# Kernel tuning notes

Measured on AMD Instinct MI355X. Metric: run time of the kernel, lower is better.

Reference implementation:

```python
import jax, jax.numpy as jnp
import numpy as np

H = 1152  # hidden_size
NH = 16   # num_attention_heads
HD = H // NH  # head_dim = 72
FF = 4304  # intermediate_size
EPS = 1e-6
S = 4096
B = 1
NDOCS = 32


def _linear_params(key, d_in, d_out):
    kw, kb = jax.random.split(key)
    lim = 1.0 / np.sqrt(d_in)
    w = jax.random.uniform(kw, (d_out, d_in), jnp.float32, -lim, lim)
    b = jax.random.uniform(kb, (d_out,), jnp.float32, -lim, lim)
    return w, b


def setup_inputs() -> dict:
    key = jax.random.key(0)
    ks = jax.random.split(key, 8)
    hidden_states = jax.random.normal(ks[0], (B, S, H), jnp.float32)
    document_ids = jnp.sort(jax.random.randint(ks[1], (S,), 0, NDOCS))
    q_w, q_b = _linear_params(ks[2], H, H)
    k_w, k_b = _linear_params(ks[3], H, H)
    v_w, v_b = _linear_params(ks[4], H, H)
    o_w, o_b = _linear_params(ks[5], H, H)
    fc1_w, fc1_b = _linear_params(ks[6], H, FF)
    fc2_w, fc2_b = _linear_params(ks[7], FF, H)
    return {
        'hidden_states': hidden_states,
        'document_ids': document_ids,
        'q_w': q_w, 'q_b': q_b, 'k_w': k_w, 'k_b': k_b,
        'v_w': v_w, 'v_b': v_b, 'o_w': o_w, 'o_b': o_b,
        'ln1_g': jnp.ones((H,), jnp.float32), 'ln1_b': jnp.zeros((H,), jnp.float32),
        'ln2_g': jnp.ones((H,), jnp.float32), 'ln2_b': jnp.zeros((H,), jnp.float32),
        'fc1_w': fc1_w, 'fc1_b': fc1_b, 'fc2_w': fc2_w, 'fc2_b': fc2_b,
    }


def _layer_norm(x, g, b):
    mu = jnp.mean(x, axis=-1, keepdims=True)
    var = jnp.mean(jnp.square(x - mu), axis=-1, keepdims=True)
    return (x - mu) * jax.lax.rsqrt(var + EPS) * g + b


def _forward(hidden_states, q_w, q_b, k_w, k_b, v_w, v_b, o_w, o_b,
             ln1_g, ln1_b, ln2_g, ln2_b, fc1_w, fc1_b, fc2_w, fc2_b,
             document_ids):
    b, s, _ = hidden_states.shape
    scale = HD ** -0.5

    residual = hidden_states
    x = _layer_norm(hidden_states, ln1_g, ln1_b)

    # projections (torch Linear: y = x @ W.T + b)
    q = (x @ q_w.T + q_b).reshape(b, s, NH, HD).transpose(0, 2, 1, 3)
    k = (x @ k_w.T + k_b).reshape(b, s, NH, HD).transpose(0, 2, 1, 3)
    v = (x @ v_w.T + v_b).reshape(b, s, NH, HD).transpose(0, 2, 1, 3)

    # document-masked attention: attend only within same document id
    scores = jnp.einsum('bhqd,bhkd->bhqk', q, k) * scale
    mask = document_ids[:, None] == document_ids[None, :]  # [s, s]
    scores = jnp.where(mask[None, None], scores, -jnp.inf)
    attn = jax.nn.softmax(scores, axis=-1)
    out = jnp.einsum('bhqk,bhkd->bhqd', attn, v)  # [b,h,s,d]
    out = out.transpose(0, 2, 1, 3).reshape(b, s, H)
    out = out @ o_w.T + o_b

    hidden = residual + out
    residual = hidden
    x = _layer_norm(hidden, ln2_g, ln2_b)
    x = jax.nn.gelu(x @ fc1_w.T + fc1_b, approximate=True)
    x = x @ fc2_w.T + fc2_b
    return residual + x


def reference(hidden_states, document_ids, q_w, q_b, k_w, k_b, v_w, v_b,
              o_w, o_b, ln1_g, ln1_b, ln2_g, ln2_b, fc1_w, fc1_b, fc2_w, fc2_b):
    return _forward(hidden_states, q_w, q_b, k_w, k_b, v_w, v_b, o_w, o_b,
                    ln1_g, ln1_b, ln2_g, ln2_b, fc1_w, fc1_b, fc2_w, fc2_b,
                    document_ids)
```

## Files before the change

kernel.cpp:

```cpp
#include <hip/hip_runtime.h>

typedef unsigned short u16;
typedef unsigned int u32;
typedef __attribute__((ext_vector_type(8))) __bf16 bf16x8;
typedef __attribute__((ext_vector_type(8))) u16 u16x8;
typedef __attribute__((ext_vector_type(4))) float f32x4;
typedef __attribute__((ext_vector_type(2))) u32 u32x2;

#define SEQ 4096
#define HID 1152
#define NHEAD 16
#define HDIM 72
#define FF 4304
#define FFP 4352
#define H3 3456

__device__ __forceinline__ u16 f2bf(float f) {
  u32 u = __builtin_bit_cast(u32, f);
  u32 r = u + 0x7fffu + ((u >> 16) & 1u);
  return (u16)(r >> 16);
}
__device__ __forceinline__ float bf2f(u16 h) {
  return __builtin_bit_cast(float, (u32)h << 16);
}
__device__ __forceinline__ float bflo(u32 u) { return __builtin_bit_cast(float, u << 16); }
__device__ __forceinline__ float bfhi(u32 u) { return __builtin_bit_cast(float, u & 0xffff0000u); }

typedef const __attribute__((address_space(1))) void* gas_t;
typedef __attribute__((address_space(3))) void* las_t;
__device__ __forceinline__ void load_lds16(const void* g, void* l) {
  __builtin_amdgcn_global_load_lds((gas_t)(unsigned long long)g,
                                   (las_t)(u32)(unsigned long long)l, 16, 0, 0);
}

__device__ __forceinline__ float gelu_fast(float x) {
  float z = 0.7978845608f * (x + 0.044715f * x * x * x);
  return x / (1.f + __expf(-2.f * z));
}

__global__ __launch_bounds__(256) void cvt4x4_k(const float* __restrict__ a,
                                                const float* __restrict__ b,
                                                const float* __restrict__ c,
                                                const float* __restrict__ d,
                                                u16* __restrict__ out, int n4) {
  int i = blockIdx.x * 256 + threadIdx.x;
  if (i >= n4) return;
  const float* in = (blockIdx.y == 0) ? a : (blockIdx.y == 1) ? b : (blockIdx.y == 2) ? c : d;
  f32x4 f = ((const f32x4*)in)[i];
  u32x2 o;
  o[0] = (u32)f2bf(f[0]) | ((u32)f2bf(f[1]) << 16);
  o[1] = (u32)f2bf(f[2]) | ((u32)f2bf(f[3]) << 16);
  ((u32x2*)(out + (size_t)blockIdx.y * n4 * 4))[i] = o;
}

__global__ __launch_bounds__(256) void cvt4_pad_k(const float* __restrict__ in,
                                                  u16* __restrict__ out,
                                                  int rows, int sc, int dc) {
  int i = blockIdx.x * 256 + threadIdx.x;
  long long n4 = (long long)rows * dc / 4;
  if (i >= n4) return;
  long long idx = (long long)i * 4;
  int r = (int)(idx / dc);
  int c = (int)(idx % dc);
  u32x2 o;
  if (c < sc) {
    f32x4 f = *(const f32x4*)(in + (size_t)r * sc + c);
    o[0] = (u32)f2bf(f[0]) | ((u32)f2bf(f[1]) << 16);
    o[1] = (u32)f2bf(f[2]) | ((u32)f2bf(f[3]) << 16);
  } else {
    o[0] = 0; o[1] = 0;
  }
  ((u32x2*)out)[i] = o;
}

__global__ __launch_bounds__(256) void prep_k(const int* __restrict__ ids,
                                              const float* __restrict__ qb,
                                              const float* __restrict__ kb,
                                              const float* __restrict__ vb,
                                              const float* __restrict__ f1b,
                                              int* __restrict__ se,
                                              float* __restrict__ bqkv,
                                              float* __restrict__ bf1,
                                              float* __restrict__ zbuf) {
  int i = blockIdx.x * 256 + threadIdx.x;
  if (i < H3) bqkv[i] = (i < HID) ? qb[i] : (i < 2 * HID ? kb[i - HID] : vb[i - 2 * HID]);
  if (i < FFP) bf1[i] = (i < FF) ? f1b[i] : 0.f;
  if (i < 16) zbuf[i] = 0.f;
  if (i < SEQ) {
    int id = ids[i];
    int lo = 0, hi = SEQ;
    while (lo < hi) { int mid = (lo + hi) >> 1; if (ids[mid] < id) lo = mid + 1; else hi = mid; }
    int s = lo;
    lo = 0; hi = SEQ;
    while (lo < hi) { int mid = (lo + hi) >> 1; if (ids[mid] <= id) lo = mid + 1; else hi = mid; }
    se[2 * i] = s;
    se[2 * i + 1] = lo;
  }
}

__global__ __launch_bounds__(256) void ln_k(const float* __restrict__ x,
                                            const float* __restrict__ g,
                                            const float* __restrict__ b,
                                            u16* __restrict__ y) {
  __shared__ float sred[8];
  int row = blockIdx.x, tid = threadIdx.x;
  const f32x4* xr = (const f32x4*)(x + (size_t)row * HID);
  f32x4 v0 = {}, v1 = {};
  float s = 0.f, s2 = 0.f;
  int c0 = tid, c1 = tid + 256;
  v0 = xr[c0];
  if (c1 < 288) v1 = xr[c1];
#pragma unroll
  for (int j = 0; j < 4; ++j) { s += v0[j] + v1[j]; s2 += v0[j] * v0[j] + v1[j] * v1[j]; }
#pragma unroll
  for (int sh = 32; sh; sh >>= 1) { s += __shfl_xor(s, sh); s2 += __shfl_xor(s2, sh); }
  if ((tid & 63) == 0) { sred[tid >> 6] = s; sred[4 + (tid >> 6)] = s2; }
  __syncthreads();
  s = sred[0] + sred[1] + sred[2] + sred[3];
  s2 = sred[4] + sred[5] + sred[6] + sred[7];
  float mu = s * (1.f / HID);
  float rs = rsqrtf(s2 * (1.f / HID) - mu * mu + 1e-6f);
  u16* yr = y + (size_t)row * HID;
  const f32x4* g4 = (const f32x4*)g;
  const f32x4* b4 = (const f32x4*)b;
  {
    f32x4 gv = g4[c0], bv = b4[c0];
    u32x2 o;
    o[0] = (u32)f2bf((v0[0] - mu) * rs * gv[0] + bv[0]) |
           ((u32)f2bf((v0[1] - mu) * rs * gv[1] + bv[1]) << 16);
    o[1] = (u32)f2bf((v0[2] - mu) * rs * gv[2] + bv[2]) |
           ((u32)f2bf((v0[3] - mu) * rs * gv[3] + bv[3]) << 16);
    *(u32x2*)(yr + c0 * 4) = o;
  }
  if (c1 < 288) {
    f32x4 gv = g4[c1], bv = b4[c1];
    u32x2 o;
    o[0] = (u32)f2bf((v1[0] - mu) * rs * gv[0] + bv[0]) |
           ((u32)f2bf((v1[1] - mu) * rs * gv[1] + bv[1]) << 16);
    o[1] = (u32)f2bf((v1[2] - mu) * rs * gv[2] + bv[2]) |
           ((u32)f2bf((v1[3] - mu) * rs * gv[3] + bv[3]) << 16);
    *(u32x2*)(yr + c1 * 4) = o;
  }
}

template <int EP>
__global__ __launch_bounds__(256, 4) void gemm_bt(const u16* __restrict__ A,
                                                  const u16* __restrict__ B,
                                                  void* __restrict__ outp,
                                                  const float* __restrict__ bias,
                                                  const float* __restrict__ resid,
                                                  int M, int N, int K) {
  __shared__ u16 As[128 * 64];
  __shared__ u16 Bs[128 * 64];
  int tid = threadIdx.x;
  int l = tid & 63, w = tid >> 6;
  int nxy = gridDim.x * gridDim.y;
  int bidf = blockIdx.y * gridDim.x + blockIdx.x;
  int cpx = nxy >> 3;
  bidf = (bidf & 7) * cpx + (bidf >> 3);
  int m0 = (bidf / gridDim.x) * 128;
  int n0 = (bidf % gridDim.x) * 128;
  int wr = w >> 1, wc = w & 1;
  f32x4 acc[4][4] = {};
  int srow = tid >> 3;
  int scol = ((tid & 7) * 16) ^ ((srow & 7) << 4);
  const char* Ab = (const char*)A + ((size_t)(m0 + srow) * K) * 2 + scol;
  const char* Bb = (const char*)B + ((size_t)(n0 + srow) * K) * 2 + scol;
  char* AsD = (char*)As + w * 1024;
  char* BsD = (char*)Bs + w * 1024;
  const char* ArB = (const char*)As + (wr * 64 + (l & 15)) * 128;
  const char* BrB = (const char*)Bs + (wc * 64 + (l & 15)) * 128;
  int c0 = ((l >> 4) * 16) ^ ((l & 7) << 4);
  int c1 = c0 ^ 64;
  int k0 = 0, kend = K;
  if (EP == 5) {
    int nz = gridDim.z;
    int ksp = ((K / 64 + nz - 1) / nz) * 64;
    k0 = blockIdx.z * ksp;
    kend = min(K, k0 + ksp);
  }
  for (int kt = k0; kt < kend; kt += 64) {
    size_t kb = (size_t)kt * 2;
#pragma unroll
    for (int i = 0; i < 4; ++i) {
      load_lds16(Ab + (size_t)i * 32 * K * 2 + kb, AsD + i * 4096);
      load_lds16(Bb + (size_t)i * 32 * K * 2 + kb, BsD + i * 4096);
    }
    __syncthreads();
#pragma unroll
    for (int kk = 0; kk < 2; ++kk) {
      int ck = kk ? c1 : c0;
      bf16x8 af[4], bfr[4];
#pragma unroll
      for (int m = 0; m < 4; ++m) af[m] = *(const bf16x8*)(ArB + m * 2048 + ck);
#pragma unroll
      for (int n = 0; n < 4; ++n) bfr[n] = *(const bf16x8*)(BrB + n * 2048 + ck);
#pragma unroll
      for (int m = 0; m < 4; ++m)
#pragma unroll
        for (int n = 0; n < 4; ++n)
          acc[m][n] = __builtin_amdgcn_mfma_f32_16x16x32_bf16(af[m], bfr[n], acc[m][n], 0, 0, 0);
    }
    __syncthreads();
  }
#pragma unroll
  for (int m = 0; m < 4; ++m) {
    int row = m0 + wr * 64 + m * 16 + (l >> 4) * 4;
#pragma unroll
    for (int n = 0; n < 4; ++n) {
      int col = n0 + wc * 64 + n * 16 + (l & 15);
      float bv = (EP == 5) ? 0.f : bias[col];
      if (EP == 4) {
        int region = (col >= 2304) ? 2 : (col >= 1152 ? 1 : 0);
        int cw = col - region * 1152;
        int hh = cw / 72;
        int dd = cw - hh * 72;
        u16* dst = (u16*)outp + (((size_t)region * NHEAD + hh) * SEQ) * HDIM + dd;
#pragma unroll
        for (int j = 0; j < 4; ++j)
          dst[(size_t)(row + j) * HDIM] = f2bf(acc[m][n][j] + bv);
      } else if (EP == 5) {
        u16* P = (u16*)outp + (size_t)blockIdx.z * M * N;
#pragma unroll
        for (int j = 0; j < 4; ++j)
          P[(size_t)(row + j) * N + col] = f2bf(acc[m][n][j]);
      } else {
#pragma unroll
        for (int j = 0; j < 4; ++j) {
          size_t idx = (size_t)(row + j) * N + col;
          float v = acc[m][n][j] + bv;
          if (EP == 1) ((u16*)outp)[idx] = f2bf(gelu_fast(v));
          else ((float*)outp)[idx] = v + resid[idx];
        }
      }
    }
  }
}

template <int NS>
__global__ __launch_bounds__(256) void splitk_reduce_k(const u16* __restrict__ P,
                                                       const float* __restrict__ bias,
                                                       const float* __restrict__ resid,
                                                       float* __restrict__ out, int n4) {
  int i = blockIdx.x * 256 + threadIdx.x;
  if (i >= n4) return;
  size_t base = (size_t)i * 4;
  int col = (int)(base % HID);
  f32x4 a = {};
#pragma unroll
  for (int s = 0; s < NS; ++s) {
    u32x2 pv = *(const u32x2*)(P + (size_t)s * SEQ * HID + base);
    a[0] += bflo(pv[0]);
    a[1] += bfhi(pv[0]);
    a[2] += bflo(pv[1]);
    a[3] += bfhi(pv[1]);
  }
  f32x4 bv = *(const f32x4*)(bias + col);
  f32x4 rv = ((const f32x4*)resid)[i];
  ((f32x4*)out)[i] = a + bv + rv;
}

__device__ __forceinline__ u32 swz(u32 a) { return a ^ (((a >> 8) & 7u) << 4); }

__global__ __launch_bounds__(256, 2) void attn_mfma_k(const u16* __restrict__ qkvh,
                                                      const int* __restrict__ se,
                                                      const float* __restrict__ zb,
                                                      u16* __restrict__ outb) {
  __shared__ u16 Ks[128 * 104];
  __shared__ u16 Vt[80 * 128];
  __shared__ u16 Ps[4][16 * 128];
  __shared__ int Sq[64], Eq[64];
  int tid = threadIdx.x, l = tid & 63, w = tid >> 6;
  int h = blockIdx.y, q0 = blockIdx.x * 64;
  const float scale = 0.1178511302f;
  const u16* Qh = qkvh + (size_t)h * SEQ * HDIM;
  const u16* Kh = qkvh + ((size_t)NHEAD + h) * SEQ * HDIM;
  const u16* Vh = qkvh + ((size_t)2 * NHEAD + h) * SEQ * HDIM;

  for (int i = tid; i < 512; i += 256) ((u32*)(Vt + 72 * 128))[i] = 0;

#pragma unroll
  for (int it = 0; it < 4; ++it) {
    int cw0 = it * 256 + w * 64;
    if (cw0 < 832) {
      int chunk = cw0 + l;
      int row = chunk / 13, c16 = chunk - row * 13;
      const void* src = (c16 < 9)
                            ? (const void*)(Qh + ((size_t)(q0 + row)) * HDIM + c16 * 8)
                            : (const void*)zb;
      load_lds16(src, (char*)Ks + (size_t)cw0 * 16);
    }
  }
  if (tid < 64) { Sq[tid] = se[2 * (q0 + tid)]; Eq[tid] = se[2 * (q0 + tid) + 1]; }
  __syncthreads();

  int sqj[4], eqj[4];
#pragma unroll
  for (int j = 0; j < 4; ++j) {
    int ql = w * 16 + (l >> 4) * 4 + j;
    sqj[j] = Sq[ql]; eqj[j] = Eq[ql];
  }
  const char* Aq = (const char*)Ks + (w * 16 + (l & 15)) * 208 + (l >> 4) * 16;
  bf16x8 aq[3];
#pragma unroll
  for (int dsl = 0; dsl < 3; ++dsl) aq[dsl] = *(const bf16x8*)(Aq + dsl * 64);
  __syncthreads();

  int kmin = se[2 * q0];
  int kmax = se[2 * (q0 + 63) + 1];
  f32x4 o[5] = {};
  float m_run[4], l_run[4];
#pragma unroll
  for (int j = 0; j < 4; ++j) { m_run[j] = -1e30f; l_run[j] = 0.f; }

  for (int kc = kmin; kc < kmax; kc += 128) {
#pragma unroll
    for (int it = 0; it < 7; ++it) {
      int cw0 = it * 256 + w * 64;
      if (cw0 < 1664) {
        int chunk = cw0 + l;
        int row = chunk / 13, c16 = chunk - row * 13;
        int krow = kc + row;
        const void* src = (c16 < 9 && krow < SEQ)
                              ? (const void*)(Kh + (size_t)krow * HDIM + c16 * 8)
                              : (const void*)zb;
        load_lds16(src, (char*)Ks + (size_t)cw0 * 16);
      }
    }
#pragma unroll
    for (int it = 0; it < 3; ++it) {
      int idx = it * 256 + tid;
      if (idx < 576) {
        int k2 = idx / 9, d8 = idx - k2 * 9;
        int kr0 = kc + 2 * k2, kr1 = kr0 + 1;
        kr0 = kr0 < SEQ ? kr0 : SEQ - 1;
        kr1 = kr1 < SEQ ? kr1 : SEQ - 1;
        u16x8 r0 = *(const u16x8*)(Vh + (size_t)kr0 * HDIM + d8 * 8);
        u16x8 r1 = *(const u16x8*)(Vh + (size_t)kr1 * HDIM + d8 * 8);
#pragma unroll
        for (int j = 0; j < 8; ++j) {
          u32 pr = (u32)r0[j] | ((u32)r1[j] << 16);
          *(u32*)((char*)Vt + swz((u32)(d8 * 8 + j) * 256 + (u32)k2 * 4)) = pr;
        }
      }
    }
    __syncthreads();

    f32x4 sf[8];
#pragma unroll
    for (int kt = 0; kt < 8; ++kt) {
      const char* Bk = (const char*)Ks + (kt * 16 + (l & 15)) * 208 + (l >> 4) * 16;
      f32x4 acc = {};
      acc = __builtin_amdgcn_mfma_f32_16x16x32_bf16(aq[0], *(const bf16x8*)Bk, acc, 0, 0, 0);
      acc = __builtin_amdgcn_mfma_f32_16x16x32_bf16(aq[1], *(const bf16x8*)(Bk + 64), acc, 0, 0, 0);
      acc = __builtin_amdgcn_mfma_f32_16x16x32_bf16(aq[2], *(const bf16x8*)(Bk + 128), acc, 0, 0, 0);
      sf[kt] = acc;
    }
    float mx[4] = {-1e30f, -1e30f, -1e30f, -1e30f};
#pragma unroll
    for (int kt = 0; kt < 8; ++kt) {
      int key = kc + kt * 16 + (l & 15);
#pragma unroll
      for (int j = 0; j < 4; ++j) {
        float s = sf[kt][j] * scale;
        bool valid = (key >= sqj[j]) && (key < eqj[j]);
        s = valid ? s : -1e30f;
        sf[kt][j] = s;
        mx[j] = fmaxf(mx[j], s);
      }
    }
#pragma unroll
    for (int j = 0; j < 4; ++j) {
      float m = mx[j];
      m = fmaxf(m, __shfl_xor(m, 1));
      m = fmaxf(m, __shfl_xor(m, 2));
      m = fmaxf(m, __shfl_xor(m, 4));
      m = fmaxf(m, __shfl_xor(m, 8));
      mx[j] = m;
    }
    float fz[4], ps[4];
#pragma unroll
    for (int j = 0; j < 4; ++j) {
      float mn = fmaxf(m_run[j], mx[j]);
      fz[j] = __expf(m_run[j] - mn);
      m_run[j] = mn;
      ps[j] = 0.f;
    }
#pragma unroll
    for (int kt = 0; kt < 8; ++kt)
#pragma unroll
      for (int j = 0; j < 4; ++j) {
        float s = sf[kt][j];
        float p = (s > -1e29f) ? __expf(s - m_run[j]) : 0.f;
        sf[kt][j] = p;
        ps[j] += p;
      }
#pragma unroll
    for (int j = 0; j < 4; ++j) {
      float p = ps[j];
      p += __shfl_xor(p, 1);
      p += __shfl_xor(p, 2);
      p += __shfl_xor(p, 4);
      p += __shfl_xor(p, 8);
      l_run[j] = l_run[j] * fz[j] + p;
#pragma unroll
      for (int dt = 0; dt < 5; ++dt) o[dt][j] *= fz[j];
    }
    char* PB = (char*)Ps[w];
#pragma unroll
    for (int kt = 0; kt < 8; ++kt)
#pragma unroll
      for (int j = 0; j < 4; ++j) {
        u32 a = (u32)((l >> 4) * 4 + j) * 256 + (u32)(kt * 16 + (l & 15)) * 2;
        *(u16*)(PB + swz(a)) = f2bf(sf[kt][j]);
      }
#pragma unroll
    for (int ks = 0; ks < 4; ++ks) {
      u32 aa = (u32)(l & 15) * 256 + (u32)((l >> 4) * 8 + ks * 32) * 2;
      bf16x8 ap = *(const bf16x8*)(PB + swz(aa));
#pragma unroll
      for (int dt = 0; dt < 5; ++dt) {
        u32 ba = (u32)(dt * 16 + (l & 15)) * 256 + (u32)((l >> 4) * 8 + ks * 32) * 2;
        bf16x8 bv = *(const bf16x8*)((const char*)Vt + swz(ba));
        o[dt] = __builtin_amdgcn_mfma_f32_16x16x32_bf16(ap, bv, o[dt], 0, 0, 0);
      }
    }
    __syncthreads();
  }

  float inv[4];
#pragma unroll
  for (int j = 0; j < 4; ++j) inv[j] = 1.f / l_run[j];
#pragma unroll
  for (int dt = 0; dt < 5; ++dt) {
    int d = dt * 16 + (l & 15);
    if (d < HDIM) {
#pragma unroll
      for (int j = 0; j < 4; ++j) {
        int q = q0 + w * 16 + (l >> 4) * 4 + j;
        outb[(size_t)q * HID + h * HDIM + d] = f2bf(o[dt][j] * inv[j]);
      }
    }
  }
}

constexpr size_t SZ_WQKV = (size_t)H3 * HID * 2;
constexpr size_t SZ_WO   = (size_t)HID * HID * 2;
constexpr size_t SZ_WF1  = (size_t)FFP * HID * 2;
constexpr size_t SZ_WF2  = (size_t)HID * FFP * 2;
constexpr size_t OFF_WQKV = 0;
constexpr size_t OFF_WO   = OFF_WQKV + SZ_WQKV;
constexpr size_t OFF_WF1  = OFF_WO + SZ_WO;
constexpr size_t OFF_BQKV = OFF_WF1 + SZ_WF1;
constexpr size_t OFF_BF1  = OFF_BQKV + (size_t)H3 * 4;
constexpr size_t OFF_SE   = OFF_BF1 + (size_t)FFP * 4;
constexpr size_t OFF_ZB   = OFF_SE + (size_t)SEQ * 2 * 4;
constexpr size_t OFF_XLN  = OFF_ZB + 64;
constexpr size_t OFF_QKV  = OFF_XLN + (size_t)SEQ * HID * 2;
constexpr size_t OFF_ACT  = OFF_QKV;
constexpr size_t OFF_AOUT = OFF_QKV + (size_t)SEQ * H3 * 2;
constexpr size_t OFF_HD   = OFF_AOUT + (size_t)SEQ * HID * 2;
constexpr size_t OFF_WF2  = OFF_HD + (size_t)SEQ * HID * 4;
constexpr size_t WS_NEED  = OFF_WF2 + SZ_WF2;
constexpr size_t OFF_P    = 0;
static_assert(OFF_ACT + (size_t)SEQ * FFP * 2 <= OFF_HD, "ACT must not clobber HD");
static_assert(3 * (size_t)SEQ * HID * 2 <= OFF_QKV, "P must stay in dead prefix");

extern "C" void kernel_launch(void* const* d_in, const int* in_sizes, int n_in,
                              void* d_out, int out_size, void* d_ws, size_t ws_size,
                              hipStream_t stream) {
  const float* hs   = (const float*)d_in[0];
  const int*   ids  = (const int*)d_in[1];
  const float* q_w  = (const float*)d_in[2];
  const float* q_b  = (const float*)d_in[3];
  const float* k_w  = (const float*)d_in[4];
  const float* k_b  = (const float*)d_in[5];
  const float* v_w  = (const float*)d_in[6];
  const float* v_b  = (const float*)d_in[7];
  const float* o_w  = (const float*)d_in[8];
  const float* o_b  = (const float*)d_in[9];
  const float* ln1g = (const float*)d_in[10];
  const float* ln1b = (const float*)d_in[11];
  const float* ln2g = (const float*)d_in[12];
  const float* ln2b = (const float*)d_in[13];
  const float* f1w  = (const float*)d_in[14];
  const float* f1b  = (const float*)d_in[15];
  const float* f2w  = (const float*)d_in[16];
  const float* f2b  = (const float*)d_in[17];

  if (ws_size < WS_NEED) return;

  char* ws = (char*)d_ws;
  u16*   Wqkv = (u16*)(ws + OFF_WQKV);
  u16*   Wf1  = (u16*)(ws + OFF_WF1);
  u16*   Wf2  = (u16*)(ws + OFF_WF2);
  float* Bqkv = (float*)(ws + OFF_BQKV);
  float* Bf1  = (float*)(ws + OFF_BF1);
  int*   SE   = (int*)(ws + OFF_SE);
  float* ZB   = (float*)(ws + OFF_ZB);
  u16*   XLN  = (u16*)(ws + OFF_XLN);
  u16*   QKVh = (u16*)(ws + OFF_QKV);
  u16*   ACT  = (u16*)(ws + OFF_ACT);
  u16*   AOUT = (u16*)(ws + OFF_AOUT);
  float* HD   = (float*)(ws + OFF_HD);
  u16*   Pp   = (u16*)(ws + OFF_P);
  u16*   Wo   = (u16*)(ws + OFF_WO);

  prep_k<<<dim3((FFP + 255) / 256), dim3(256), 0, stream>>>(ids, q_b, k_b, v_b, f1b, SE, Bqkv,
                                                            Bf1, ZB);
  int nW = HID * HID;
  cvt4x4_k<<<dim3(nW / 4 / 256, 4), dim3(256), 0, stream>>>(q_w, k_w, v_w, o_w, Wqkv, nW / 4);
  {
    int n4 = FFP * HID / 4;
    cvt4_pad_k<<<dim3((n4 + 255) / 256), dim3(256), 0, stream>>>(f1w, Wf1, 1, FF * HID, FFP * HID);
  }
  {
    int n4 = HID * FFP / 4;
    cvt4_pad_k<<<dim3((n4 + 255) / 256), dim3(256), 0, stream>>>(f2w, Wf2, HID, FF, FFP);
  }

  ln_k<<<dim3(SEQ), dim3(256), 0, stream>>>(hs, ln1g, ln1b, XLN);
  gemm_bt<4><<<dim3(H3 / 128, SEQ / 128), dim3(256), 0, stream>>>(XLN, Wqkv, QKVh, Bqkv, nullptr,
                                                                  SEQ, H3, HID);
  attn_mfma_k<<<dim3(SEQ / 64, NHEAD), dim3(256), 0, stream>>>(QKVh, SE, ZB, AOUT);
  gemm_bt<2><<<dim3(HID / 128, SEQ / 128), dim3(256), 0, stream>>>(AOUT, Wo, HD, o_b, hs,
                                                                   SEQ, HID, HID);
  ln_k<<<dim3(SEQ), dim3(256), 0, stream>>>(HD, ln2g, ln2b, XLN);
  gemm_bt<1><<<dim3(FFP / 128, SEQ / 128), dim3(256), 0, stream>>>(XLN, Wf1, ACT, Bf1, nullptr,
                                                                   SEQ, FFP, HID);
  gemm_bt<5><<<dim3(HID / 128, SEQ / 128, 3), dim3(256), 0, stream>>>(ACT, Wf2, Pp, nullptr,
                                                                      nullptr, SEQ, HID, FFP);
  splitk_reduce_k<3><<<dim3(SEQ * HID / 4 / 256), dim3(256), 0, stream>>>(Pp, f2b, HD,
                                                                          (float*)d_out,
                                                                          SEQ * HID / 4);
}
```

Before: 293.2 us.

## Triple-buffer GEMM LDS tiles with K=32 steps and async prefetch two ahead

Restructures the bt GEMM main loop to use three LDS buffers of 32-wide K slices. Global-to-LDS loads for step t+2 are issued before computing step t, with explicit vmcnt waits and raw barriers, so memory latency overlaps MFMA work. A new XOR swizzle is applied for the 64-byte rows. Occupancy hint drops from 4 to 3 blocks, and each step now has half the K work per barrier pair, so barrier overhead per unit of work goes up.

```diff
diff --git a/kernel.cpp b/kernel.cpp
--- a/kernel.cpp
+++ b/kernel.cpp
@@ -144,14 +144,14 @@
 }
 
 template <int EP>
-__global__ __launch_bounds__(256, 4) void gemm_bt(const u16* __restrict__ A,
+__global__ __launch_bounds__(256, 3) void gemm_bt(const u16* __restrict__ A,
                                                   const u16* __restrict__ B,
                                                   void* __restrict__ outp,
                                                   const float* __restrict__ bias,
                                                   const float* __restrict__ resid,
                                                   int M, int N, int K) {
-  __shared__ u16 As[128 * 64];
-  __shared__ u16 Bs[128 * 64];
+  __shared__ u16 As[3 * 128 * 32];
+  __shared__ u16 Bs[3 * 128 * 32];
   int tid = threadIdx.x;
   int l = tid & 63, w = tid >> 6;
   int nxy = gridDim.x * gridDim.y;
@@ -162,46 +162,74 @@
   int n0 = (bidf % gridDim.x) * 128;
   int wr = w >> 1, wc = w & 1;
   f32x4 acc[4][4] = {};
-  int srow = tid >> 3;
-  int scol = ((tid & 7) * 16) ^ ((srow & 7) << 4);
-  const char* Ab = (const char*)A + ((size_t)(m0 + srow) * K) * 2 + scol;
-  const char* Bb = (const char*)B + ((size_t)(n0 + srow) * K) * 2 + scol;
-  char* AsD = (char*)As + w * 1024;
-  char* BsD = (char*)Bs + w * 1024;
-  const char* ArB = (const char*)As + (wr * 64 + (l & 15)) * 128;
-  const char* BrB = (const char*)Bs + (wc * 64 + (l & 15)) * 128;
-  int c0 = ((l >> 4) * 16) ^ ((l & 7) << 4);
-  int c1 = c0 ^ 64;
+  int sr = tid >> 2, sc = tid & 3;
+  int row0 = sr, row1 = 64 + sr;
+  int x0 = ((row0 >> 1) & 3) ^ (((row0 >> 3) & 1) << 1);
+  int x1 = ((row1 >> 1) & 3) ^ (((row1 >> 3) & 1) << 1);
+  const char* Ag0 = (const char*)A + ((size_t)(m0 + row0) * K + (size_t)((sc ^ x0) * 8)) * 2;
+  const char* Ag1 = (const char*)A + ((size_t)(m0 + row1) * K + (size_t)((sc ^ x1) * 8)) * 2;
+  const char* Bg0 = (const char*)B + ((size_t)(n0 + row0) * K + (size_t)((sc ^ x0) * 8)) * 2;
+  const char* Bg1 = (const char*)B + ((size_t)(n0 + row1) * K + (size_t)((sc ^ x1) * 8)) * 2;
+  char* AsB = (char*)As;
+  char* BsB = (char*)Bs;
+  int xl = (((l & 15) >> 1) & 3) ^ ((((l & 15) >> 3) & 1) << 1);
+  int cfr = ((l >> 4) ^ xl) * 16;
+  const char* ArB = (const char*)As + (wr * 64 + (l & 15)) * 64 + cfr;
+  const char* BrB = (const char*)Bs + (wc * 64 + (l & 15)) * 64 + cfr;
   int k0 = 0, kend = K;
   if (EP == 5) {
     int nz = gridDim.z;
-    int ksp = ((K / 64 + nz - 1) / nz) * 64;
+    int ksp = ((K / 32 + nz - 1) / nz) * 32;
     k0 = blockIdx.z * ksp;
     kend = min(K, k0 + ksp);
   }
-  for (int kt = k0; kt < kend; kt += 64) {
-    size_t kb = (size_t)kt * 2;
-#pragma unroll
-    for (int i = 0; i < 4; ++i) {
-      load_lds16(Ab + (size_t)i * 32 * K * 2 + kb, AsD + i * 4096);
-      load_lds16(Bb + (size_t)i * 32 * K * 2 + kb, BsD + i * 4096);
-    }
-    __syncthreads();
-#pragma unroll
-    for (int kk = 0; kk < 2; ++kk) {
-      int ck = kk ? c1 : c0;
+  int nsteps = (kend - k0) / 32;
+  {
+    size_t kb0 = (size_t)k0 * 2;
+    load_lds16(Ag0 + kb0, AsB + tid * 16);
+    load_lds16(Ag1 + kb0, AsB + 4096 + tid * 16);
+    load_lds16(Bg0 + kb0, BsB + tid * 16);
+    load_lds16(Bg1 + kb0, BsB + 4096 + tid * 16);
+    size_t kb1 = (size_t)(k0 + 32) * 2;
+    load_lds16(Ag0 + kb1, AsB + 8192 + tid * 16);
+    load_lds16(Ag1 + kb1, AsB + 8192 + 4096 + tid * 16);
+    load_lds16(Bg0 + kb1, BsB + 8192 + tid * 16);
+    load_lds16(Bg1 + kb1, BsB + 8192 + 4096 + tid * 16);
+  }
+  int buf = 0;
+  for (int t = 0; t < nsteps; ++t) {
+    if (t + 2 < nsteps) {
+      int nb = buf >= 1 ? buf - 1 : 2;
+      size_t kb = (size_t)(k0 + (t + 2) * 32) * 2;
+      load_lds16(Ag0 + kb, AsB + nb * 8192 + tid * 16);
+      load_lds16(Ag1 + kb, AsB + nb * 8192 + 4096 + tid * 16);
+      load_lds16(Bg0 + kb, BsB + nb * 8192 + tid * 16);
+      load_lds16(Bg1 + kb, BsB + nb * 8192 + 4096 + tid * 16);
+      asm volatile("s_waitcnt vmcnt(4)" ::: "memory");
+    } else {
+      asm volatile("s_waitcnt vmcnt(0)" ::: "memory");
+    }
+    __builtin_amdgcn_sched_barrier(0);
+    __builtin_amdgcn_s_barrier();
+    __builtin_amdgcn_sched_barrier(0);
+    {
+      const char* Ar = ArB + buf * 8192;
+      const char* Br = BrB + buf * 8192;
       bf16x8 af[4], bfr[4];
 #pragma unroll
-      for (int m = 0; m < 4; ++m) af[m] = *(const bf16x8*)(ArB + m * 2048 + ck);
-#pragma unroll
-      for (int n = 0; n < 4; ++n) bfr[n] = *(const bf16x8*)(BrB + n * 2048 + ck);
+      for (int m = 0; m < 4; ++m) af[m] = *(const bf16x8*)(Ar + m * 1024);
+#pragma unroll
+      for (int n = 0; n < 4; ++n) bfr[n] = *(const bf16x8*)(Br + n * 1024);
 #pragma unroll
       for (int m = 0; m < 4; ++m)
 #pragma unroll
         for (int n = 0; n < 4; ++n)
           acc[m][n] = __builtin_amdgcn_mfma_f32_16x16x32_bf16(af[m], bfr[n], acc[m][n], 0, 0, 0);
     }
-    __syncthreads();
+    __builtin_amdgcn_sched_barrier(0);
+    __builtin_amdgcn_s_barrier();
+    __builtin_amdgcn_sched_barrier(0);
+    buf = buf == 2 ? 0 : buf + 1;
   }
 #pragma unroll
   for (int m = 0; m < 4; ++m) {
```

New measurement: 286.2 us. 1.02x faster.

## Triple-buffer B tiles in LDS and load A fragments directly from global

Applied to the files above, without the earlier changes.

The GEMM now loads the A operand fragments straight from global memory into registers instead of staging them through shared memory. The B tile is kept in a three-deep LDS ring buffer so that loads run two k-steps ahead of the MFMA work, with manual vmcnt waits and barriers. The aim is to overlap global loads with compute and to remove the full-tile synchronisation stall. In exchange the kernel uses more LDS (occupancy bound lowered to 3), issues uncoalesced per-lane global reads for A, and correctness now relies on exact vmcnt accounting. It also assumes the K range is a multiple of 64 with at least two steps.

```diff
diff --git a/kernel.cpp b/kernel.cpp
--- a/kernel.cpp
+++ b/kernel.cpp
@@ -144,14 +144,13 @@
 }
 
 template <int EP>
-__global__ __launch_bounds__(256, 4) void gemm_bt(const u16* __restrict__ A,
+__global__ __launch_bounds__(256, 3) void gemm_bt(const u16* __restrict__ A,
                                                   const u16* __restrict__ B,
                                                   void* __restrict__ outp,
                                                   const float* __restrict__ bias,
                                                   const float* __restrict__ resid,
                                                   int M, int N, int K) {
-  __shared__ u16 As[128 * 64];
-  __shared__ u16 Bs[128 * 64];
+  __shared__ u16 Bs[3 * 128 * 64];
   int tid = threadIdx.x;
   int l = tid & 63, w = tid >> 6;
   int nxy = gridDim.x * gridDim.y;
@@ -164,14 +163,13 @@
   f32x4 acc[4][4] = {};
   int srow = tid >> 3;
   int scol = ((tid & 7) * 16) ^ ((srow & 7) << 4);
-  const char* Ab = (const char*)A + ((size_t)(m0 + srow) * K) * 2 + scol;
   const char* Bb = (const char*)B + ((size_t)(n0 + srow) * K) * 2 + scol;
-  char* AsD = (char*)As + w * 1024;
-  char* BsD = (char*)Bs + w * 1024;
-  const char* ArB = (const char*)As + (wr * 64 + (l & 15)) * 128;
+  const u16* Arow[4];
+#pragma unroll
+  for (int m = 0; m < 4; ++m)
+    Arow[m] = A + (size_t)(m0 + wr * 64 + m * 16 + (l & 15)) * K + (l >> 4) * 8;
   const char* BrB = (const char*)Bs + (wc * 64 + (l & 15)) * 128;
   int c0 = ((l >> 4) * 16) ^ ((l & 7) << 4);
-  int c1 = c0 ^ 64;
   int k0 = 0, kend = K;
   if (EP == 5) {
     int nz = gridDim.z;
@@ -179,29 +177,57 @@
     k0 = blockIdx.z * ksp;
     kend = min(K, k0 + ksp);
   }
-  for (int kt = k0; kt < kend; kt += 64) {
-    size_t kb = (size_t)kt * 2;
-#pragma unroll
-    for (int i = 0; i < 4; ++i) {
-      load_lds16(Ab + (size_t)i * 32 * K * 2 + kb, AsD + i * 4096);
-      load_lds16(Bb + (size_t)i * 32 * K * 2 + kb, BsD + i * 4096);
-    }
-    __syncthreads();
-#pragma unroll
-    for (int kk = 0; kk < 2; ++kk) {
-      int ck = kk ? c1 : c0;
-      bf16x8 af[4], bfr[4];
-#pragma unroll
-      for (int m = 0; m < 4; ++m) af[m] = *(const bf16x8*)(ArB + m * 2048 + ck);
-#pragma unroll
-      for (int n = 0; n < 4; ++n) bfr[n] = *(const bf16x8*)(BrB + n * 2048 + ck);
-#pragma unroll
-      for (int m = 0; m < 4; ++m)
-#pragma unroll
-        for (int n = 0; n < 4; ++n)
-          acc[m][n] = __builtin_amdgcn_mfma_f32_16x16x32_bf16(af[m], bfr[n], acc[m][n], 0, 0, 0);
-    }
-    __syncthreads();
+  int nsteps = (kend - k0) / 64;
+#pragma unroll
+  for (int tt = 0; tt < 2; ++tt) {
+    size_t kb = (size_t)(k0 + tt * 64) * 2;
+#pragma unroll
+    for (int i = 0; i < 4; ++i)
+      load_lds16(Bb + (size_t)(i * 32) * K * 2 + kb, (char*)Bs + tt * 16384 + w * 1024 + i * 4096);
+  }
+  int buf = 0;
+  for (int t = 0; t < nsteps; ++t) {
+    bf16x8 af[4][2];
+    size_t ka = (size_t)(k0 + t * 64);
+#pragma unroll
+    for (int m = 0; m < 4; ++m)
+#pragma unroll
+      for (int kk = 0; kk < 2; ++kk)
+        af[m][kk] = *(const bf16x8*)(Arow[m] + ka + kk * 32);
+    if (t + 2 < nsteps) {
+      int nb = buf >= 1 ? buf - 1 : 2;
+      size_t kb = (size_t)(k0 + (t + 2) * 64) * 2;
+#pragma unroll
+      for (int i = 0; i < 4; ++i)
+        load_lds16(Bb + (size_t)(i * 32) * K * 2 + kb,
+                   (char*)Bs + nb * 16384 + w * 1024 + i * 4096);
+      asm volatile("s_waitcnt vmcnt(12)" ::: "memory");
+    } else {
+      asm volatile("s_waitcnt vmcnt(8)" ::: "memory");
+    }
+    __builtin_amdgcn_sched_barrier(0);
+    __builtin_amdgcn_s_barrier();
+    __builtin_amdgcn_sched_barrier(0);
+    {
+      const char* Br = BrB + buf * 16384;
+#pragma unroll
+      for (int kk = 0; kk < 2; ++kk) {
+        int ck = c0 ^ (kk * 64);
+        bf16x8 bfr[4];
+#pragma unroll
+        for (int n = 0; n < 4; ++n) bfr[n] = *(const bf16x8*)(Br + n * 16 * 128 + ck);
+#pragma unroll
+        for (int m = 0; m < 4; ++m)
+#pragma unroll
+          for (int n = 0; n < 4; ++n)
+            acc[m][n] =
+                __builtin_amdgcn_mfma_f32_16x16x32_bf16(af[m][kk], bfr[n], acc[m][n], 0, 0, 0);
+      }
+    }
+    __builtin_amdgcn_sched_barrier(0);
+    __builtin_amdgcn_s_barrier();
+    __builtin_amdgcn_sched_barrier(0);
+    buf = buf == 2 ? 0 : buf + 1;
   }
 #pragma unroll
   for (int m = 0; m < 4; ++m) {
```

After: 438.5 us. 49.5% more time.
